# Kernel optimization log

Measured on AMD Instinct MI355X. Metric: run time of the kernel, lower is better.

The kernel has to match this reference:

```python
import jax, jax.numpy as jnp
import numpy as np

NUM_CLASSES = 10000
FEAT_DIM = 1024
BATCH = 4096


def setup_inputs() -> dict:
    key = jax.random.key(0)
    k1, k2 = jax.random.split(key)
    feat = jax.random.normal(k1, (BATCH, FEAT_DIM), dtype=jnp.float32)
    centers = jax.random.normal(k2, (NUM_CLASSES, FEAT_DIM), dtype=jnp.float32)
    return {"feat": feat, "centers": centers}


def reference(feat, centers):
    # logits = -0.5 * ||feat_b - center_c||^2, computed via the GEMM rewrite
    # ||a-b||^2 = ||a||^2 + ||b||^2 - 2 a.b  (same math as broadcast-sub-square-sum,
    # but avoids the [B, C, D] intermediate and uses tensor-core matmul).
    feat_sq = jnp.sum(feat * feat, axis=-1, keepdims=True)          # [B, 1]
    cent_sq = jnp.sum(centers * centers, axis=-1)[None, :]          # [1, C]
    cross = jnp.einsum('bd,cd->bc', feat, centers)                  # [B, C]
    dist = feat_sq + cent_sq - 2.0 * cross                          # [B, C]
    logits = -0.5 * dist
    return logits
```

## Files before the change

kernel.cpp:

```cpp
#include <hip/hip_runtime.h>
#include <hip/hip_bf16.h>
#include <stdint.h>

#define M_DIM 4096
#define N_DIM 10000
#define K_DIM 1024

typedef __attribute__((ext_vector_type(8))) short bf16x8;
typedef __attribute__((ext_vector_type(4))) float f32x4;

__device__ __forceinline__ void async_ld16(const void* g, void* l) {
    __builtin_amdgcn_global_load_lds(
        (const __attribute__((address_space(1))) unsigned int*)g,
        (__attribute__((address_space(3))) unsigned int*)l,
        16, 0, 0);
}

__device__ __forceinline__ unsigned short f2bf(float f) {
    unsigned u = __float_as_uint(f);
    unsigned r = (u + 0x7FFFu + ((u >> 16) & 1u)) >> 16;
    return (unsigned short)r;
}

__global__ __launch_bounds__(256) void prep_rows(
    const float* __restrict__ in, unsigned short* __restrict__ outb,
    float* __restrict__ sq)
{
    const int row = blockIdx.x;
    const int t = threadIdx.x;
    const float4* ip = (const float4*)(in + (size_t)row * K_DIM);
    float4 v = ip[t];
    ushort4 pk;
    pk.x = f2bf(v.x); pk.y = f2bf(v.y); pk.z = f2bf(v.z); pk.w = f2bf(v.w);
    ((ushort4*)(outb + (size_t)row * K_DIM))[t] = pk;
    float s = v.x * v.x + v.y * v.y + v.z * v.z + v.w * v.w;
    #pragma unroll
    for (int off = 32; off > 0; off >>= 1) s += __shfl_down(s, off, 64);
    __shared__ float ws[4];
    if ((t & 63) == 0) ws[t >> 6] = s;
    __syncthreads();
    if (t == 0) sq[row] = ws[0] + ws[1] + ws[2] + ws[3];
}

__global__ __launch_bounds__(256) void gemm_bt(
    const unsigned short* __restrict__ A,
    const unsigned short* __restrict__ B,
    const float* __restrict__ fsq, const float* __restrict__ csq,
    float* __restrict__ out)
{
    __shared__ unsigned short As[128 * 32];
    __shared__ unsigned short Bs[128 * 32];

    const int tid  = threadIdx.x;
    const int lane = tid & 63;
    const int wave = tid >> 6;
    const int wm = wave & 1, wn = wave >> 1;
    const int bm = blockIdx.y, bn = blockIdx.x;

    const int arow_base = bm * 128;
    const int brow_base = bn * 128;

    const int srow = tid >> 2;
    const int scol = (tid & 3) * 8;

    const unsigned short* gA0 = A + (size_t)(arow_base + srow) * K_DIM + scol;
    const unsigned short* gA1 = gA0 + (size_t)64 * K_DIM;
    int br0 = brow_base + srow;      if (br0 > N_DIM - 1) br0 = N_DIM - 1;
    int br1 = brow_base + 64 + srow; if (br1 > N_DIM - 1) br1 = N_DIM - 1;
    const unsigned short* gB0 = B + (size_t)br0 * K_DIM + scol;
    const unsigned short* gB1 = B + (size_t)br1 * K_DIM + scol;

    unsigned short* lA0 = As + tid * 8;
    unsigned short* lA1 = As + 2048 + tid * 8;
    unsigned short* lB0 = Bs + tid * 8;
    unsigned short* lB1 = Bs + 2048 + tid * 8;

    f32x4 acc[4][4];
    #pragma unroll
    for (int i = 0; i < 4; i++)
        #pragma unroll
        for (int j = 0; j < 4; j++) {
            f32x4 z = {0.f, 0.f, 0.f, 0.f};
            acc[i][j] = z;
        }

    const int mlane = lane & 15;
    const int quad  = lane >> 4;

    const unsigned short* aptr = As + (wm * 64 + mlane) * 32 + quad * 8;
    const unsigned short* bptr = Bs + (wn * 64 + mlane) * 32 + quad * 8;

    for (int kt = 0; kt < K_DIM / 32; ++kt) {
        async_ld16(gA0, lA0);
        async_ld16(gA1, lA1);
        async_ld16(gB0, lB0);
        async_ld16(gB1, lB1);
        gA0 += 32; gA1 += 32; gB0 += 32; gB1 += 32;
        __syncthreads();

        bf16x8 af[4], bfv[4];
        #pragma unroll
        for (int i = 0; i < 4; i++) {
            af[i]  = *(const bf16x8*)(aptr + i * 16 * 32);
            bfv[i] = *(const bf16x8*)(bptr + i * 16 * 32);
        }
        #pragma unroll
        for (int i = 0; i < 4; i++)
            #pragma unroll
            for (int j = 0; j < 4; j++)
                acc[i][j] = __builtin_amdgcn_mfma_f32_16x16x32_bf16(
                    af[i], bfv[j], acc[i][j], 0, 0, 0);
        __syncthreads();
    }

    const int rbase = arow_base + wm * 64 + quad * 4;
    const int cbase = brow_base + wn * 64 + mlane;
    #pragma unroll
    for (int i = 0; i < 4; i++) {
        float frow[4];
        #pragma unroll
        for (int r = 0; r < 4; r++)
            frow[r] = -0.5f * fsq[rbase + i * 16 + r];
        #pragma unroll
        for (int j = 0; j < 4; j++) {
            int col = cbase + j * 16;
            if (col < N_DIM) {
                float cs = -0.5f * csq[col];
                #pragma unroll
                for (int r = 0; r < 4; r++) {
                    int row = rbase + i * 16 + r;
                    out[(size_t)row * N_DIM + col] = acc[i][j][r] + frow[r] + cs;
                }
            }
        }
    }
}

extern "C" void kernel_launch(void* const* d_in, const int* in_sizes, int n_in,
                              void* d_out, int out_size, void* d_ws, size_t ws_size,
                              hipStream_t stream) {
    const float* feat = (const float*)d_in[0];
    const float* cent = (const float*)d_in[1];
    float* out = (float*)d_out;

    char* ws = (char*)d_ws;
    unsigned short* featbf = (unsigned short*)ws;
    unsigned short* centbf = (unsigned short*)(ws + 8388608);
    float* fsq = (float*)(ws + 8388608 + 20480000);
    float* csq = (float*)(ws + 8388608 + 20480000 + 16384);

    prep_rows<<<M_DIM, 256, 0, stream>>>(feat, featbf, fsq);
    prep_rows<<<N_DIM, 256, 0, stream>>>(cent, centbf, csq);

    dim3 grid((N_DIM + 127) / 128, M_DIM / 128);
    gemm_bt<<<grid, 256, 0, stream>>>(featbf, centbf, fsq, csq, out);
}
```

Baseline: 336.8 us.

## Fuse prep launches, swizzle GEMM tiles into column bands, use nontemporal stores

Merges the two row-preparation launches into one grid covering both feat and centers rows, removing one launch and its tail. Remaps the GEMM grid to a 1D index that walks bands of 16 N-tiles across all M-tiles, so a band's B (centers) tiles stay resident in L2 while A tiles stream past. Writes the large fp32 output with nontemporal stores so it does not evict operand data from cache. The tile swizzle costs a few integer divisions per block, and the nontemporal hint may behave differently than expected on this hardware.

Result: faster. 308.9 us (-8.3%).

```diff
diff --git a/kernel.cpp b/kernel.cpp
--- a/kernel.cpp
+++ b/kernel.cpp
@@ -5,6 +5,9 @@
 #define M_DIM 4096
 #define N_DIM 10000
 #define K_DIM 1024
+#define GM (M_DIM / 128)
+#define GN ((N_DIM + 127) / 128)
+#define SB 16
 
 typedef __attribute__((ext_vector_type(8))) short bf16x8;
 typedef __attribute__((ext_vector_type(4))) float f32x4;
@@ -23,23 +26,36 @@
 }
 
 __global__ __launch_bounds__(256) void prep_rows(
-    const float* __restrict__ in, unsigned short* __restrict__ outb,
-    float* __restrict__ sq)
+    const float* __restrict__ feat, const float* __restrict__ cent,
+    unsigned short* __restrict__ featbf, unsigned short* __restrict__ centbf,
+    float* __restrict__ fsq, float* __restrict__ csq)
 {
     const int row = blockIdx.x;
     const int t = threadIdx.x;
-    const float4* ip = (const float4*)(in + (size_t)row * K_DIM);
-    float4 v = ip[t];
+    const float* in;
+    unsigned short* outb;
+    float* sqp;
+    if (row < M_DIM) {
+        in = feat + (size_t)row * K_DIM;
+        outb = featbf + (size_t)row * K_DIM;
+        sqp = fsq + row;
+    } else {
+        const int r2 = row - M_DIM;
+        in = cent + (size_t)r2 * K_DIM;
+        outb = centbf + (size_t)r2 * K_DIM;
+        sqp = csq + r2;
+    }
+    float4 v = ((const float4*)in)[t];
     ushort4 pk;
     pk.x = f2bf(v.x); pk.y = f2bf(v.y); pk.z = f2bf(v.z); pk.w = f2bf(v.w);
-    ((ushort4*)(outb + (size_t)row * K_DIM))[t] = pk;
+    ((ushort4*)outb)[t] = pk;
     float s = v.x * v.x + v.y * v.y + v.z * v.z + v.w * v.w;
     #pragma unroll
     for (int off = 32; off > 0; off >>= 1) s += __shfl_down(s, off, 64);
     __shared__ float ws[4];
     if ((t & 63) == 0) ws[t >> 6] = s;
     __syncthreads();
-    if (t == 0) sq[row] = ws[0] + ws[1] + ws[2] + ws[3];
+    if (t == 0) *sqp = ws[0] + ws[1] + ws[2] + ws[3];
 }
 
 __global__ __launch_bounds__(256) void gemm_bt(
@@ -55,7 +71,14 @@
     const int lane = tid & 63;
     const int wave = tid >> 6;
     const int wm = wave & 1, wn = wave >> 1;
-    const int bm = blockIdx.y, bn = blockIdx.x;
+
+    const int lin  = blockIdx.x;
+    const int band = lin / (SB * GM);
+    const int r0   = lin - band * (SB * GM);
+    const int bn0  = band * SB;
+    int bw = GN - bn0; if (bw > SB) bw = SB;
+    const int bm = r0 / bw;
+    const int bn = bn0 + (r0 - bm * bw);
 
     const int arow_base = bm * 128;
     const int brow_base = bn * 128;
@@ -129,7 +152,8 @@
                 #pragma unroll
                 for (int r = 0; r < 4; r++) {
                     int row = rbase + i * 16 + r;
-                    out[(size_t)row * N_DIM + col] = acc[i][j][r] + frow[r] + cs;
+                    float v = acc[i][j][r] + frow[r] + cs;
+                    __builtin_nontemporal_store(v, &out[(size_t)row * N_DIM + col]);
                 }
             }
         }
@@ -149,9 +173,7 @@
     float* fsq = (float*)(ws + 8388608 + 20480000);
     float* csq = (float*)(ws + 8388608 + 20480000 + 16384);
 
-    prep_rows<<<M_DIM, 256, 0, stream>>>(feat, featbf, fsq);
-    prep_rows<<<N_DIM, 256, 0, stream>>>(cent, centbf, csq);
+    prep_rows<<<M_DIM + N_DIM, 256, 0, stream>>>(feat, cent, featbf, centbf, fsq, csq);
 
-    dim3 grid((N_DIM + 127) / 128, M_DIM / 128);
-    gemm_bt<<<grid, 256, 0, stream>>>(featbf, centbf, fsq, csq, out);
+    gemm_bt<<<GM * GN, 256, 0, stream>>>(featbf, centbf, fsq, csq, out);
 }
```
